# Kernel optimization log

Hardware: AMD Instinct MI355X
Metric: run time of the kernel (lower is better)

Reference implementation:

```python
import jax, jax.numpy as jnp
import numpy as np

CLS_NUM = 16
SCALE = 8.0
STRIDE = 5
NO_OBJ_SCALE = 1.0
EPS = 1e-7


def setup_inputs() -> dict:
    key = jax.random.key(0)
    k1, k2, k3, k4, k5, k6, k7, k8 = jax.random.split(key, 8)
    nB, nH, nW = 16, 160, 160
    N = 2048
    predict = jax.random.normal(k1, (nB, 6 + CLS_NUM, nH, nW), dtype=jnp.float32)
    b = jax.random.randint(k2, (N,), 0, nB).astype(jnp.float32)
    c = jax.random.randint(k3, (N,), 0, CLS_NUM).astype(jnp.float32)
    cx = jax.random.uniform(k4, (N,), minval=0.0, maxval=nW * SCALE)
    cy = jax.random.uniform(k5, (N,), minval=0.0, maxval=nH * SCALE)
    w = jax.random.uniform(k6, (N,), minval=8.0, maxval=80.0)
    h = jax.random.uniform(k7, (N,), minval=8.0, maxval=80.0)
    ang = jax.random.uniform(k8, (N,), minval=-np.pi, maxval=np.pi)
    targets = jnp.stack([b, c, cx, cy, w, h, ang], axis=-1).astype(jnp.float32)
    return {"predict": predict, "targets": targets}


def _masks(targets, nB, nH, nW):
    """Vectorized render_map/build_heatmap: per-(class,batch) obj / noobj grid masks."""
    b_idx = targets[:, 0].astype(jnp.int32)
    c_idx = targets[:, 1].astype(jnp.int32)
    cx = targets[:, 2] / SCALE
    cy = targets[:, 3] / SCALE
    w = targets[:, 4] / SCALE
    h = targets[:, 5] / SCALE
    ang = targets[:, 6]
    cos, sin = jnp.cos(ang), jnp.sin(ang)
    xr = cx * cos + cy * sin          # rotated box center
    yr = -cx * sin + cy * cos
    x3, x4 = xr - h / 2, xr + h / 2   # tight bounds
    y3, y4 = yr - w / 2, yr + w / 2
    x1, x2 = x3 - 0.5, x4 + 0.5       # widened bounds (noobj clearing)
    y1, y2 = y3 - 0.5, y4 + 0.5
    gx = jnp.arange(nW, dtype=jnp.float32) + 0.5   # [W]
    gy = jnp.arange(nH, dtype=jnp.float32) + 0.5   # [H]
    # rotated grid coords per box: [N, H, W]
    vx = cos[:, None, None] * gx[None, None, :] + sin[:, None, None] * gy[None, :, None]
    vy = -sin[:, None, None] * gx[None, None, :] + cos[:, None, None] * gy[None, :, None]

    def inside(xl, xh, yl, yh):
        m = (xl[:, None, None] <= vx) & (vx <= xh[:, None, None]) \
            & (yl[:, None, None] <= vy) & (vy <= yh[:, None, None])
        return m.astype(jnp.float32)

    obj_n = inside(x3, x4, y3, y4)    # [N, H, W]
    wide_n = inside(x1, x2, y1, y2)
    seg = c_idx * nB + b_idx
    nseg = CLS_NUM * nB
    obj_sum = jax.ops.segment_sum(obj_n, seg, num_segments=nseg).reshape(CLS_NUM, nB, nH, nW)
    wide_sum = jax.ops.segment_sum(wide_n, seg, num_segments=nseg).reshape(CLS_NUM, nB, nH, nW)
    obj_mask = obj_sum > 0
    noobj_mask = wide_sum == 0
    return obj_mask, noobj_mask


def reference(predict, targets):
    nB, C, nH, nW = predict.shape
    pred = jnp.transpose(predict, (0, 2, 3, 1))  # [B, H, W, C]
    half = (STRIDE - 1) / 2
    x = jax.nn.sigmoid(pred[..., 0]) * STRIDE - half
    y = jax.nn.sigmoid(pred[..., 1]) * STRIDE - half
    w = pred[..., 2]
    h = pred[..., 3]
    p = jax.nn.sigmoid(pred[..., 4]) * 2 - 1
    q = jax.nn.sigmoid(pred[..., 5]) * 2 - 1

    # ---- confidence loss (per class, BCE on obj / noobj cells) ----
    obj_mask, noobj_mask = _masks(targets, nB, nH, nW)     # [Cls, B, H, W]
    conf = jax.nn.sigmoid(jnp.transpose(pred[..., 6:], (3, 0, 1, 2)))  # [Cls, B, H, W]
    confc = jnp.clip(conf, EPS, 1.0 - EPS)
    obj_f = obj_mask.astype(conf.dtype)
    noobj_f = noobj_mask.astype(conf.dtype)
    n_obj = jnp.sum(obj_f, axis=(1, 2, 3))
    n_noobj = jnp.sum(noobj_f, axis=(1, 2, 3))
    loss_obj = jnp.sum(obj_f * (-jnp.log(confc)), axis=(1, 2, 3)) / jnp.maximum(n_obj, 1.0)
    loss_noobj = jnp.sum(noobj_f * (-jnp.log(1.0 - confc)), axis=(1, 2, 3)) / jnp.maximum(n_noobj, 1.0)
    per_cls = jnp.where(n_obj > 0, loss_obj + NO_OBJ_SCALE * loss_noobj, 0.0)
    loss = jnp.sum(per_cls)

    # ---- box decoding (eval output) ----
    score = jax.nn.sigmoid(pred[..., 6:])
    conf_max = jnp.max(score, axis=-1)
    cls_id = jnp.argmax(score, axis=-1).astype(pred.dtype)
    grid_x = jnp.broadcast_to(jnp.arange(nW, dtype=pred.dtype)[None, None, :], (nB, nH, nW))
    grid_y = jnp.broadcast_to(jnp.arange(nH, dtype=pred.dtype)[None, :, None], (nB, nH, nW))
    t = jnp.sqrt((1 + p) / 2 + 1e-16)
    bang = jnp.arctan2(q / (2 * t + 1e-16), t)
    boxes = jnp.stack([
        conf_max,
        cls_id,
        (grid_x + x) * SCALE,
        (grid_y + y) * SCALE,
        jnp.exp(w) * SCALE,
        jnp.exp(h) * SCALE,
        bang,
    ], axis=-1)                      # [B, H, W, 7]
    output = boxes.reshape(nB, nH * nW, 7)
    return (loss, output)
```

## Files before the change

kernel.cpp:

```cpp
#include <hip/hip_runtime.h>
#include <math.h>

#define CLS_NUM 16
#define NB 16
#define NH 160
#define NW 160
#define NCH 22
#define CSZ 25600
#define NT 2048
#define TPB 256
#define NBOXU 1600
#define NMASKU 2560
#define CAP 256
#define EPS_F 1e-7f


__global__ __launch_bounds__(TPB) void detect_main(
        const float* __restrict__ predict,
        const float* __restrict__ targets,
        float* __restrict__ out,
        float* __restrict__ partial)
{
    __shared__ float tg[CAP][6];
    __shared__ float red_s[16];
    __shared__ int cnt_s;

    const int tid = threadIdx.x;
    const int bid = blockIdx.x;

    if (bid < NBOXU) {
        int b = bid / 100;
        int r = (bid % 100) * TPB + tid;
        const float* pb = predict + (size_t)b * NCH * CSZ + r;
        float p0 = pb[0];
        float p1 = pb[1 * CSZ];
        float p2 = pb[2 * CSZ];
        float p3 = pb[3 * CSZ];
        float p4 = pb[4 * CSZ];
        float p5 = pb[5 * CSZ];
        float bestraw = pb[6 * CSZ];
        int bi = 0;
        #pragma unroll
        for (int cc = 1; cc < CLS_NUM; cc++) {
            float v = pb[(6 + cc) * CSZ];
            if (v > bestraw) { bestraw = v; bi = cc; }
        }
        float x = 1.0f / (1.0f + __expf(-p0)) * 5.0f - 2.0f;
        float y = 1.0f / (1.0f + __expf(-p1)) * 5.0f - 2.0f;
        float p = 1.0f / (1.0f + __expf(-p4)) * 2.0f - 1.0f;
        float q = 1.0f / (1.0f + __expf(-p5)) * 2.0f - 1.0f;
        float best = 1.0f / (1.0f + __expf(-bestraw));
        float tq = sqrtf((1.0f + p) * 0.5f + 1e-16f);
        float bang = atan2f(q / (2.0f * tq + 1e-16f), tq);
        int i = r / NW, j = r % NW;
        float* o = out + 1 + ((size_t)b * CSZ + r) * 7;
        o[0] = best;
        o[1] = (float)bi;
        o[2] = ((float)j + x) * 8.0f;
        o[3] = ((float)i + y) * 8.0f;
        o[4] = __expf(p2) * 8.0f;
        o[5] = __expf(p3) * 8.0f;
        o[6] = bang;
        return;
    }

    const int u = bid - NBOXU;
    const int pair = u / 10, tile = u - pair * 10;
    const int c = pair >> 4, b = pair & 15;
    const int rb = tile * 16;

    if (tid == 0) cnt_s = 0;
    __syncthreads();

    const float rbc = (float)rb + 8.0f;
    const float rlo = (float)rb + 0.5f, rhi = (float)rb + 15.5f;

    for (int n = tid; n < NT; n += TPB) {
        const float* tp = targets + n * 7;
        if ((int)tp[0] == b && (int)tp[1] == c) {
            float cx = tp[2] * 0.125f, cy = tp[3] * 0.125f;
            float w  = tp[4] * 0.125f, h  = tp[5] * 0.125f;
            float R = 0.5f * sqrtf(w * w + h * h) + 0.75f;
            if (cy + R >= rlo && cy - R <= rhi) {
                float ang = tp[6];
                float cs_ = cosf(ang), sn_ = sinf(ang);
                float xr =  cx * cs_ + cy * sn_;
                float yr = -cx * sn_ + cy * cs_;
                float x3 = xr - h * 0.5f, x4 = xr + h * 0.5f;
                float y3 = yr - w * 0.5f, y4 = yr + w * 0.5f;
                float acs = fabsf(cs_), asn = fabsf(sn_);
                float ex = acs * 79.5f + asn * 7.5f + 1e-3f;
                float ey = acs * 7.5f  + asn * 79.5f + 1e-3f;
                float vxc = cs_ * 80.0f + sn_ * rbc;
                float vyc = cs_ * rbc   - sn_ * 80.0f;
                if (!(vxc + ex < x3 - 0.5f || vxc - ex > x4 + 0.5f ||
                      vyc + ey < y3 - 0.5f || vyc - ey > y4 + 0.5f)) {
                    int slot = atomicAdd(&cnt_s, 1);
                    if (slot < CAP) {
                        tg[slot][0] = cs_; tg[slot][1] = sn_;
                        tg[slot][2] = x3;  tg[slot][3] = x4;
                        tg[slot][4] = y3;  tg[slot][5] = y4;
                    }
                }
            }
        }
    }
    __syncthreads();
    const int cnt = min(cnt_s, CAP);

    float gx[10], gy[10];
    #pragma unroll
    for (int k = 0; k < 10; k++) {
        int cell = tid + k * TPB;
        gx[k] = (float)(cell % NW) + 0.5f;
        gy[k] = (float)(rb + cell / NW) + 0.5f;
    }

    unsigned objb = 0, wideb = 0;
    for (int t = 0; t < cnt; t++) {
        float cs_ = tg[t][0], sn_ = tg[t][1];
        float x3 = tg[t][2], x4 = tg[t][3], y3 = tg[t][4], y4 = tg[t][5];
        #pragma unroll
        for (int k = 0; k < 10; k++) {
            float vx = cs_ * gx[k] + sn_ * gy[k];
            float vy = cs_ * gy[k] - sn_ * gx[k];
            float mn = fminf(fminf(vx - x3, x4 - vx),
                             fminf(vy - y3, y4 - vy));
            objb  |= (mn >= 0.0f)  ? (1u << k) : 0u;
            wideb |= (mn >= -0.5f) ? (1u << k) : 0u;
        }
    }

    const float* cp = predict + ((size_t)(b * NCH + 6 + c)) * CSZ + rb * NW;
    float ao = 0.f, an = 0.f;
    #pragma unroll
    for (int k = 0; k < 10; k++) {
        float pv = cp[tid + k * TPB];
        float s  = 1.0f / (1.0f + __expf(-pv));
        float sc = fminf(fmaxf(s, EPS_F), 1.0f - EPS_F);
        if ((objb >> k) & 1u)     ao -= __logf(sc);
        if (!((wideb >> k) & 1u)) an -= __logf(1.0f - sc);
    }
    float co = (float)__popc(objb);
    float cn = (float)__popc(~wideb & 0x3FFu);
    #pragma unroll
    for (int o = 32; o > 0; o >>= 1) {
        ao += __shfl_down(ao, o);
        an += __shfl_down(an, o);
        co += __shfl_down(co, o);
        cn += __shfl_down(cn, o);
    }
    if ((tid & 63) == 0) {
        int wid = tid >> 6;
        red_s[wid * 4 + 0] = ao; red_s[wid * 4 + 1] = an;
        red_s[wid * 4 + 2] = co; red_s[wid * 4 + 3] = cn;
    }
    __syncthreads();
    if (tid < 4) {
        float s = red_s[tid] + red_s[4 + tid] + red_s[8 + tid] + red_s[12 + tid];
        partial[u * 4 + tid] = s;
    }
}

__global__ __launch_bounds__(256) void finalize_kernel(
        const float* __restrict__ partial,
        float* __restrict__ out)
{
    __shared__ float fin_s[4][64];
    int tid = threadIdx.x;
    int v = tid & 63, g = tid >> 6;
    int c2 = v >> 2, comp = v & 3;
    float s = 0.f;
    for (int i = 0; i < 40; i++)
        s += partial[(c2 * 160 + g * 40 + i) * 4 + comp];
    fin_s[g][v] = s;
    __syncthreads();
    if (tid < 64)
        fin_s[0][tid] = fin_s[0][tid] + fin_s[1][tid] + fin_s[2][tid] + fin_s[3][tid];
    __syncthreads();
    if (tid == 0) {
        float L = 0.f;
        for (int c = 0; c < CLS_NUM; c++) {
            float ao = fin_s[0][c * 4 + 0], an = fin_s[0][c * 4 + 1];
            float co = fin_s[0][c * 4 + 2], cn = fin_s[0][c * 4 + 3];
            if (co > 0.f) L += ao / fmaxf(co, 1.f) + an / fmaxf(cn, 1.f);
        }
        out[0] = L;
    }
}

extern "C" void kernel_launch(void* const* d_in, const int* in_sizes, int n_in,
                              void* d_out, int out_size, void* d_ws, size_t ws_size,
                              hipStream_t stream) {
    const float* predict = (const float*)d_in[0];
    const float* targets = (const float*)d_in[1];
    float* out = (float*)d_out;
    float* partial = (float*)d_ws;

    detect_main<<<NBOXU + NMASKU, TPB, 0, stream>>>(predict, targets, out, partial);
    finalize_kernel<<<1, 256, 0, stream>>>(partial, out);
}
```

Measured before the change: 41.58 us.

## Fold noobj loss into box-decode pass and sparsify mask blocks across classes

```diff
diff --git a/kernel.cpp b/kernel.cpp
--- a/kernel.cpp
+++ b/kernel.cpp
@@ -10,7 +10,9 @@
 #define NT 2048
 #define TPB 256
 #define NBOXU 1600
-#define NMASKU 2560
+#define TILES 40
+#define NMASKU 640
+#define TCELLS 640
 #define CAP 256
 #define EPS_F 1e-7f
 
@@ -19,16 +21,17 @@
         const float* __restrict__ predict,
         const float* __restrict__ targets,
         float* __restrict__ out,
-        float* __restrict__ partial)
+        float* __restrict__ streamP,
+        float* __restrict__ maskP)
 {
-    __shared__ float tg[CAP][6];
-    __shared__ float red_s[16];
-    __shared__ int cnt_s;
-
     const int tid = threadIdx.x;
     const int bid = blockIdx.x;
 
     if (bid < NBOXU) {
+        __shared__ float acc_b[16];
+        if (tid < 16) acc_b[tid] = 0.f;
+        __syncthreads();
+
         int b = bid / 100;
         int r = (bid % 100) * TPB + tid;
         const float* pb = predict + (size_t)b * NCH * CSZ + r;
@@ -38,13 +41,25 @@
         float p3 = pb[3 * CSZ];
         float p4 = pb[4 * CSZ];
         float p5 = pb[5 * CSZ];
-        float bestraw = pb[6 * CSZ];
-        int bi = 0;
-        #pragma unroll
-        for (int cc = 1; cc < CLS_NUM; cc++) {
-            float v = pb[(6 + cc) * CSZ];
-            if (v > bestraw) { bestraw = v; bi = cc; }
-        }
+        float raw[16];
+        #pragma unroll
+        for (int cc = 0; cc < CLS_NUM; cc++) raw[cc] = pb[(6 + cc) * CSZ];
+
+        float bestraw = raw[0]; int bi = 0;
+        #pragma unroll
+        for (int cc = 1; cc < CLS_NUM; cc++)
+            if (raw[cc] > bestraw) { bestraw = raw[cc]; bi = cc; }
+
+        #pragma unroll
+        for (int cc = 0; cc < CLS_NUM; cc++) {
+            float s  = 1.0f / (1.0f + __expf(-raw[cc]));
+            float sc = fminf(fmaxf(s, EPS_F), 1.0f - EPS_F);
+            float v  = -__logf(1.0f - sc);
+            #pragma unroll
+            for (int o = 32; o > 0; o >>= 1) v += __shfl_down(v, o);
+            if ((tid & 63) == 0) atomicAdd(&acc_b[cc], v);
+        }
+
         float x = 1.0f / (1.0f + __expf(-p0)) * 5.0f - 2.0f;
         float y = 1.0f / (1.0f + __expf(-p1)) * 5.0f - 2.0f;
         float p = 1.0f / (1.0f + __expf(-p4)) * 2.0f - 1.0f;
@@ -61,27 +76,36 @@
         o[4] = __expf(p2) * 8.0f;
         o[5] = __expf(p3) * 8.0f;
         o[6] = bang;
+
+        __syncthreads();
+        if (tid < 16) streamP[bid * 16 + tid] = acc_b[tid];
         return;
     }
 
+    __shared__ float tg[CAP][8];
+    __shared__ float acc_s[64];
+    __shared__ int cnt_s, pres_s;
+
     const int u = bid - NBOXU;
-    const int pair = u / 10, tile = u - pair * 10;
-    const int c = pair >> 4, b = pair & 15;
-    const int rb = tile * 16;
-
-    if (tid == 0) cnt_s = 0;
-    __syncthreads();
-
-    const float rbc = (float)rb + 8.0f;
-    const float rlo = (float)rb + 0.5f, rhi = (float)rb + 15.5f;
+    const int b = u / TILES;
+    const int tile = u - b * TILES;
+    const int rb = tile * 4;
+
+    if (tid == 0) { cnt_s = 0; pres_s = 0; }
+    if (tid < 64) acc_s[tid] = 0.f;
+    __syncthreads();
+
+    const float rlo = (float)rb + 0.5f, rhi = (float)rb + 3.5f;
+    const float rbc = (float)rb + 2.0f;
 
     for (int n = tid; n < NT; n += TPB) {
         const float* tp = targets + n * 7;
-        if ((int)tp[0] == b && (int)tp[1] == c) {
-            float cx = tp[2] * 0.125f, cy = tp[3] * 0.125f;
-            float w  = tp[4] * 0.125f, h  = tp[5] * 0.125f;
+        if ((int)tp[0] == b) {
+            float cy = tp[3] * 0.125f;
+            float w  = tp[4] * 0.125f, h = tp[5] * 0.125f;
             float R = 0.5f * sqrtf(w * w + h * h) + 0.75f;
             if (cy + R >= rlo && cy - R <= rhi) {
+                float cx = tp[2] * 0.125f;
                 float ang = tp[6];
                 float cs_ = cosf(ang), sn_ = sinf(ang);
                 float xr =  cx * cs_ + cy * sn_;
@@ -89,8 +113,8 @@
                 float x3 = xr - h * 0.5f, x4 = xr + h * 0.5f;
                 float y3 = yr - w * 0.5f, y4 = yr + w * 0.5f;
                 float acs = fabsf(cs_), asn = fabsf(sn_);
-                float ex = acs * 79.5f + asn * 7.5f + 1e-3f;
-                float ey = acs * 7.5f  + asn * 79.5f + 1e-3f;
+                float ex = acs * 79.5f + asn * 1.5f + 1e-3f;
+                float ey = acs * 1.5f  + asn * 79.5f + 1e-3f;
                 float vxc = cs_ * 80.0f + sn_ * rbc;
                 float vyc = cs_ * rbc   - sn_ * 80.0f;
                 if (!(vxc + ex < x3 - 0.5f || vxc - ex > x4 + 0.5f ||
@@ -100,6 +124,7 @@
                         tg[slot][0] = cs_; tg[slot][1] = sn_;
                         tg[slot][2] = x3;  tg[slot][3] = x4;
                         tg[slot][4] = y3;  tg[slot][5] = y4;
+                        tg[slot][6] = tp[1];
                     }
                 }
             }
@@ -108,82 +133,115 @@
     __syncthreads();
     const int cnt = min(cnt_s, CAP);
 
-    float gx[10], gy[10];
+    float gxa[3], gya[3];
     #pragma unroll
-    for (int k = 0; k < 10; k++) {
+    for (int k = 0; k < 3; k++) {
         int cell = tid + k * TPB;
-        gx[k] = (float)(cell % NW) + 0.5f;
-        gy[k] = (float)(rb + cell / NW) + 0.5f;
-    }
-
-    unsigned objb = 0, wideb = 0;
+        gxa[k] = (float)(cell % NW) + 0.5f;
+        gya[k] = (float)(rb + cell / NW) + 0.5f;
+    }
+    unsigned m[3] = {0u, 0u, 0u};
     for (int t = 0; t < cnt; t++) {
         float cs_ = tg[t][0], sn_ = tg[t][1];
         float x3 = tg[t][2], x4 = tg[t][3], y3 = tg[t][4], y4 = tg[t][5];
-        #pragma unroll
-        for (int k = 0; k < 10; k++) {
-            float vx = cs_ * gx[k] + sn_ * gy[k];
-            float vy = cs_ * gy[k] - sn_ * gx[k];
-            float mn = fminf(fminf(vx - x3, x4 - vx),
-                             fminf(vy - y3, y4 - vy));
-            objb  |= (mn >= 0.0f)  ? (1u << k) : 0u;
-            wideb |= (mn >= -0.5f) ? (1u << k) : 0u;
-        }
-    }
-
-    const float* cp = predict + ((size_t)(b * NCH + 6 + c)) * CSZ + rb * NW;
-    float ao = 0.f, an = 0.f;
+        int cl = (int)tg[t][6];
+        #pragma unroll
+        for (int k = 0; k < 3; k++) {
+            float vx = cs_ * gxa[k] + sn_ * gya[k];
+            float vy = cs_ * gya[k] - sn_ * gxa[k];
+            float mn = fminf(fminf(vx - x3, x4 - vx), fminf(vy - y3, y4 - vy));
+            unsigned add = (mn >= 0.0f ? 1u : 0u) | (mn >= -0.5f ? 0x10000u : 0u);
+            m[k] |= add << cl;
+        }
+    }
+    if (tid >= TCELLS - 2 * TPB) m[2] = 0u;
+
+    unsigned any = m[0] | m[1] | m[2];
     #pragma unroll
-    for (int k = 0; k < 10; k++) {
-        float pv = cp[tid + k * TPB];
-        float s  = 1.0f / (1.0f + __expf(-pv));
-        float sc = fminf(fmaxf(s, EPS_F), 1.0f - EPS_F);
-        if ((objb >> k) & 1u)     ao -= __logf(sc);
-        if (!((wideb >> k) & 1u)) an -= __logf(1.0f - sc);
-    }
-    float co = (float)__popc(objb);
-    float cn = (float)__popc(~wideb & 0x3FFu);
-    #pragma unroll
-    for (int o = 32; o > 0; o >>= 1) {
-        ao += __shfl_down(ao, o);
-        an += __shfl_down(an, o);
-        co += __shfl_down(co, o);
-        cn += __shfl_down(cn, o);
-    }
-    if ((tid & 63) == 0) {
-        int wid = tid >> 6;
-        red_s[wid * 4 + 0] = ao; red_s[wid * 4 + 1] = an;
-        red_s[wid * 4 + 2] = co; red_s[wid * 4 + 3] = cn;
-    }
-    __syncthreads();
-    if (tid < 4) {
-        float s = red_s[tid] + red_s[4 + tid] + red_s[8 + tid] + red_s[12 + tid];
-        partial[u * 4 + tid] = s;
-    }
+    for (int o = 32; o > 0; o >>= 1) any |= (unsigned)__shfl_down((int)any, o);
+    if ((tid & 63) == 0) atomicOr(&pres_s, (int)any);
+    __syncthreads();
+    const unsigned pres = (unsigned)pres_s;
+
+    const float* basec = predict + ((size_t)b * NCH + 6) * CSZ + rb * NW;
+    for (int c = 0; c < CLS_NUM; c++) {
+        if (!(pres & (0x10000u << c))) continue;
+        const float* cp = basec + (size_t)c * CSZ;
+        float ao = 0.f, no = 0.f, wsub = 0.f, wc = 0.f;
+        #pragma unroll
+        for (int k = 0; k < 3; k++) {
+            int cell = tid + k * TPB;
+            bool ob = (m[k] >> c) & 1u;
+            bool wb = (m[k] >> (16 + c)) & 1u;
+            if ((ob | wb) && cell < TCELLS) {
+                float pv = cp[cell];
+                float s  = 1.0f / (1.0f + __expf(-pv));
+                float sc = fminf(fmaxf(s, EPS_F), 1.0f - EPS_F);
+                if (ob) { ao -= __logf(sc);        no += 1.0f; }
+                if (wb) { wsub -= __logf(1.0f - sc); wc += 1.0f; }
+            }
+        }
+        #pragma unroll
+        for (int o = 32; o > 0; o >>= 1) {
+            ao   += __shfl_down(ao, o);
+            no   += __shfl_down(no, o);
+            wsub += __shfl_down(wsub, o);
+            wc   += __shfl_down(wc, o);
+        }
+        if ((tid & 63) == 0) {
+            atomicAdd(&acc_s[c * 4 + 0], ao);
+            atomicAdd(&acc_s[c * 4 + 1], no);
+            atomicAdd(&acc_s[c * 4 + 2], wsub);
+            atomicAdd(&acc_s[c * 4 + 3], wc);
+        }
+    }
+    __syncthreads();
+    if (tid < 64) maskP[u * 64 + tid] = acc_s[tid];
 }
 
 __global__ __launch_bounds__(256) void finalize_kernel(
-        const float* __restrict__ partial,
+        const float* __restrict__ streamP,
+        const float* __restrict__ maskP,
         float* __restrict__ out)
 {
-    __shared__ float fin_s[4][64];
+    __shared__ float st[16][16];
+    __shared__ float mt[4][64];
+    __shared__ float S[16];
+    __shared__ float M[64];
     int tid = threadIdx.x;
-    int v = tid & 63, g = tid >> 6;
-    int c2 = v >> 2, comp = v & 3;
-    float s = 0.f;
-    for (int i = 0; i < 40; i++)
-        s += partial[(c2 * 160 + g * 40 + i) * 4 + comp];
-    fin_s[g][v] = s;
-    __syncthreads();
-    if (tid < 64)
-        fin_s[0][tid] = fin_s[0][tid] + fin_s[1][tid] + fin_s[2][tid] + fin_s[3][tid];
+    {   int g = tid >> 4, c = tid & 15;
+        float s = 0.f;
+        for (int blk = g * 100; blk < g * 100 + 100; blk++)
+            s += streamP[blk * 16 + c];
+        st[g][c] = s;
+    }
+    {   int g = tid >> 6, v = tid & 63;
+        float s = 0.f;
+        for (int uu = g; uu < NMASKU; uu += 4) s += maskP[uu * 64 + v];
+        mt[g][v] = s;
+    }
+    __syncthreads();
+    if (tid < 64) M[tid] = mt[0][tid] + mt[1][tid] + mt[2][tid] + mt[3][tid];
+    if (tid >= 64 && tid < 80) {
+        int c = tid - 64;
+        float s = 0.f;
+        #pragma unroll
+        for (int g = 0; g < 16; g++) s += st[g][c];
+        S[c] = s;
+    }
     __syncthreads();
     if (tid == 0) {
         float L = 0.f;
         for (int c = 0; c < CLS_NUM; c++) {
-            float ao = fin_s[0][c * 4 + 0], an = fin_s[0][c * 4 + 1];
-            float co = fin_s[0][c * 4 + 2], cn = fin_s[0][c * 4 + 3];
-            if (co > 0.f) L += ao / fmaxf(co, 1.f) + an / fmaxf(cn, 1.f);
+            float ao   = M[c * 4 + 0];
+            float no   = M[c * 4 + 1];
+            float wsub = M[c * 4 + 2];
+            float wc   = M[c * 4 + 3];
+            if (no > 0.f) {
+                float nnoobj = 409600.0f - wc;
+                L += ao / fmaxf(no, 1.0f)
+                   + (S[c] - wsub) / fmaxf(nnoobj, 1.0f);
+            }
         }
         out[0] = L;
     }
@@ -195,8 +253,11 @@
     const float* predict = (const float*)d_in[0];
     const float* targets = (const float*)d_in[1];
     float* out = (float*)d_out;
-    float* partial = (float*)d_ws;
-
-    detect_main<<<NBOXU + NMASKU, TPB, 0, stream>>>(predict, targets, out, partial);
-    finalize_kernel<<<1, 256, 0, stream>>>(partial, out);
+
+    float* streamP = (float*)d_ws;
+    float* maskP   = streamP + NBOXU * 16;
+
+    detect_main<<<NBOXU + NMASKU, TPB, 0, stream>>>(predict, targets, out,
+                                                    streamP, maskP);
+    finalize_kernel<<<1, 256, 0, stream>>>(streamP, maskP, out);
 }
```

New measurement: 82.46 us. 98.3% more time.

## Fuse box decoding and per-class mask loss into one banded kernel

Applied to the files above, without the earlier changes.

```diff
diff --git a/kernel.cpp b/kernel.cpp
--- a/kernel.cpp
+++ b/kernel.cpp
@@ -8,80 +8,44 @@
 #define NCH 22
 #define CSZ 25600
 #define NT 2048
-#define TPB 256
-#define NBOXU 1600
-#define NMASKU 2560
+#define TPB 320
+#define BANDS 40
+#define NU 640
+#define BCELLS 640
 #define CAP 256
 #define EPS_F 1e-7f
 
 
-__global__ __launch_bounds__(TPB) void detect_main(
+__global__ __launch_bounds__(TPB) void detect_unified(
         const float* __restrict__ predict,
         const float* __restrict__ targets,
         float* __restrict__ out,
-        float* __restrict__ partial)
+        float* __restrict__ maskP)
 {
-    __shared__ float tg[CAP][6];
-    __shared__ float red_s[16];
+    __shared__ float tg[CAP][8];
+    __shared__ float acc_s[64];
     __shared__ int cnt_s;
 
     const int tid = threadIdx.x;
-    const int bid = blockIdx.x;
-
-    if (bid < NBOXU) {
-        int b = bid / 100;
-        int r = (bid % 100) * TPB + tid;
-        const float* pb = predict + (size_t)b * NCH * CSZ + r;
-        float p0 = pb[0];
-        float p1 = pb[1 * CSZ];
-        float p2 = pb[2 * CSZ];
-        float p3 = pb[3 * CSZ];
-        float p4 = pb[4 * CSZ];
-        float p5 = pb[5 * CSZ];
-        float bestraw = pb[6 * CSZ];
-        int bi = 0;
-        #pragma unroll
-        for (int cc = 1; cc < CLS_NUM; cc++) {
-            float v = pb[(6 + cc) * CSZ];
-            if (v > bestraw) { bestraw = v; bi = cc; }
-        }
-        float x = 1.0f / (1.0f + __expf(-p0)) * 5.0f - 2.0f;
-        float y = 1.0f / (1.0f + __expf(-p1)) * 5.0f - 2.0f;
-        float p = 1.0f / (1.0f + __expf(-p4)) * 2.0f - 1.0f;
-        float q = 1.0f / (1.0f + __expf(-p5)) * 2.0f - 1.0f;
-        float best = 1.0f / (1.0f + __expf(-bestraw));
-        float tq = sqrtf((1.0f + p) * 0.5f + 1e-16f);
-        float bang = atan2f(q / (2.0f * tq + 1e-16f), tq);
-        int i = r / NW, j = r % NW;
-        float* o = out + 1 + ((size_t)b * CSZ + r) * 7;
-        o[0] = best;
-        o[1] = (float)bi;
-        o[2] = ((float)j + x) * 8.0f;
-        o[3] = ((float)i + y) * 8.0f;
-        o[4] = __expf(p2) * 8.0f;
-        o[5] = __expf(p3) * 8.0f;
-        o[6] = bang;
-        return;
-    }
-
-    const int u = bid - NBOXU;
-    const int pair = u / 10, tile = u - pair * 10;
-    const int c = pair >> 4, b = pair & 15;
-    const int rb = tile * 16;
+    const int u   = blockIdx.x;
+    const int b   = u / BANDS;
+    const int band = u - b * BANDS;
+    const int rb  = band * 4;
 
     if (tid == 0) cnt_s = 0;
-    __syncthreads();
-
-    const float rbc = (float)rb + 8.0f;
-    const float rlo = (float)rb + 0.5f, rhi = (float)rb + 15.5f;
-
+    if (tid < 64) acc_s[tid] = 0.f;
+    __syncthreads();
+
+    const float rlo = (float)rb + 0.5f, rhi = (float)rb + 3.5f;
+    const float rbc = (float)rb + 2.0f;
     for (int n = tid; n < NT; n += TPB) {
         const float* tp = targets + n * 7;
-        if ((int)tp[0] == b && (int)tp[1] == c) {
-            float cx = tp[2] * 0.125f, cy = tp[3] * 0.125f;
-            float w  = tp[4] * 0.125f, h  = tp[5] * 0.125f;
+        if ((int)tp[0] == b) {
+            float cy = tp[3] * 0.125f;
+            float w  = tp[4] * 0.125f, h = tp[5] * 0.125f;
             float R = 0.5f * sqrtf(w * w + h * h) + 0.75f;
             if (cy + R >= rlo && cy - R <= rhi) {
+                float cx = tp[2] * 0.125f;
                 float ang = tp[6];
                 float cs_ = cosf(ang), sn_ = sinf(ang);
                 float xr =  cx * cs_ + cy * sn_;
@@ -89,8 +53,8 @@
                 float x3 = xr - h * 0.5f, x4 = xr + h * 0.5f;
                 float y3 = yr - w * 0.5f, y4 = yr + w * 0.5f;
                 float acs = fabsf(cs_), asn = fabsf(sn_);
-                float ex = acs * 79.5f + asn * 7.5f + 1e-3f;
-                float ey = acs * 7.5f  + asn * 79.5f + 1e-3f;
+                float ex = acs * 79.5f + asn * 1.5f + 1e-3f;
+                float ey = acs * 1.5f  + asn * 79.5f + 1e-3f;
                 float vxc = cs_ * 80.0f + sn_ * rbc;
                 float vyc = cs_ * rbc   - sn_ * 80.0f;
                 if (!(vxc + ex < x3 - 0.5f || vxc - ex > x4 + 0.5f ||
@@ -100,6 +64,7 @@
                         tg[slot][0] = cs_; tg[slot][1] = sn_;
                         tg[slot][2] = x3;  tg[slot][3] = x4;
                         tg[slot][4] = y3;  tg[slot][5] = y4;
+                        tg[slot][6] = tp[1];
                     }
                 }
             }
@@ -108,82 +73,122 @@
     __syncthreads();
     const int cnt = min(cnt_s, CAP);
 
-    float gx[10], gy[10];
+    unsigned m0 = 0u, m1 = 0u;
+    {
+        float gx0 = (float)(tid % NW) + 0.5f;
+        float gy0 = (float)(rb + tid / NW) + 0.5f;
+        int cell1 = tid + TPB;
+        float gx1 = (float)(cell1 % NW) + 0.5f;
+        float gy1 = (float)(rb + cell1 / NW) + 0.5f;
+        for (int t = 0; t < cnt; t++) {
+            float cs_ = tg[t][0], sn_ = tg[t][1];
+            float x3 = tg[t][2], x4 = tg[t][3], y3 = tg[t][4], y4 = tg[t][5];
+            int cl = (int)tg[t][6];
+            float vx0 = cs_ * gx0 + sn_ * gy0;
+            float vy0 = cs_ * gy0 - sn_ * gx0;
+            float mn0 = fminf(fminf(vx0 - x3, x4 - vx0), fminf(vy0 - y3, y4 - vy0));
+            m0 |= ((mn0 >= 0.0f ? 1u : 0u) | (mn0 >= -0.5f ? 0x10000u : 0u)) << cl;
+            float vx1 = cs_ * gx1 + sn_ * gy1;
+            float vy1 = cs_ * gy1 - sn_ * gx1;
+            float mn1 = fminf(fminf(vx1 - x3, x4 - vx1), fminf(vy1 - y3, y4 - vy1));
+            m1 |= ((mn1 >= 0.0f ? 1u : 0u) | (mn1 >= -0.5f ? 0x10000u : 0u)) << cl;
+        }
+    }
+
+    const float* pbase = predict + (size_t)b * NCH * CSZ + rb * NW;
+    float anS[16];
     #pragma unroll
-    for (int k = 0; k < 10; k++) {
-        int cell = tid + k * TPB;
-        gx[k] = (float)(cell % NW) + 0.5f;
-        gy[k] = (float)(rb + cell / NW) + 0.5f;
-    }
-
-    unsigned objb = 0, wideb = 0;
-    for (int t = 0; t < cnt; t++) {
-        float cs_ = tg[t][0], sn_ = tg[t][1];
-        float x3 = tg[t][2], x4 = tg[t][3], y3 = tg[t][4], y4 = tg[t][5];
+    for (int c = 0; c < CLS_NUM; c++) anS[c] = 0.f;
+
+    #pragma unroll
+    for (int k = 0; k < 2; k++) {
+        const unsigned mk = k ? m1 : m0;
+        const int cell = tid + k * TPB;
+        float bestraw = -INFINITY;
+        int bi = 0;
         #pragma unroll
-        for (int k = 0; k < 10; k++) {
-            float vx = cs_ * gx[k] + sn_ * gy[k];
-            float vy = cs_ * gy[k] - sn_ * gx[k];
-            float mn = fminf(fminf(vx - x3, x4 - vx),
-                             fminf(vy - y3, y4 - vy));
-            objb  |= (mn >= 0.0f)  ? (1u << k) : 0u;
-            wideb |= (mn >= -0.5f) ? (1u << k) : 0u;
-        }
-    }
-
-    const float* cp = predict + ((size_t)(b * NCH + 6 + c)) * CSZ + rb * NW;
-    float ao = 0.f, an = 0.f;
+        for (int c = 0; c < CLS_NUM; c++) {
+            float pv = pbase[(size_t)(6 + c) * CSZ + cell];
+            if (pv > bestraw) { bestraw = pv; bi = c; }
+            float s  = 1.0f / (1.0f + __expf(-pv));
+            float sc = fminf(fmaxf(s, EPS_F), 1.0f - EPS_F);
+            float lnn = -__logf(1.0f - sc);
+            bool wb = (mk >> (16 + c)) & 1u;
+            bool ob = (mk >> c) & 1u;
+            anS[c] += wb ? 0.f : lnn;
+            if (ob) {
+                atomicAdd(&acc_s[c * 4 + 0], -__logf(sc));
+                atomicAdd(&acc_s[c * 4 + 1], 1.0f);
+            }
+            if (wb) atomicAdd(&acc_s[c * 4 + 3], 1.0f);
+        }
+        float p0 = pbase[cell];
+        float p1 = pbase[(size_t)1 * CSZ + cell];
+        float p2 = pbase[(size_t)2 * CSZ + cell];
+        float p3 = pbase[(size_t)3 * CSZ + cell];
+        float p4 = pbase[(size_t)4 * CSZ + cell];
+        float p5 = pbase[(size_t)5 * CSZ + cell];
+        float x = 1.0f / (1.0f + __expf(-p0)) * 5.0f - 2.0f;
+        float y = 1.0f / (1.0f + __expf(-p1)) * 5.0f - 2.0f;
+        float p = 1.0f / (1.0f + __expf(-p4)) * 2.0f - 1.0f;
+        float q = 1.0f / (1.0f + __expf(-p5)) * 2.0f - 1.0f;
+        float best = 1.0f / (1.0f + __expf(-bestraw));
+        float tq = sqrtf((1.0f + p) * 0.5f + 1e-16f);
+        float bang = atan2f(q / (2.0f * tq + 1e-16f), tq);
+        int i = rb + cell / NW, j = cell % NW;
+        float* o = out + 1 + ((size_t)b * CSZ + (size_t)i * NW + j) * 7;
+        o[0] = best;
+        o[1] = (float)bi;
+        o[2] = ((float)j + x) * 8.0f;
+        o[3] = ((float)i + y) * 8.0f;
+        o[4] = __expf(p2) * 8.0f;
+        o[5] = __expf(p3) * 8.0f;
+        o[6] = bang;
+    }
+
     #pragma unroll
-    for (int k = 0; k < 10; k++) {
-        float pv = cp[tid + k * TPB];
-        float s  = 1.0f / (1.0f + __expf(-pv));
-        float sc = fminf(fmaxf(s, EPS_F), 1.0f - EPS_F);
-        if ((objb >> k) & 1u)     ao -= __logf(sc);
-        if (!((wideb >> k) & 1u)) an -= __logf(1.0f - sc);
-    }
-    float co = (float)__popc(objb);
-    float cn = (float)__popc(~wideb & 0x3FFu);
-    #pragma unroll
-    for (int o = 32; o > 0; o >>= 1) {
-        ao += __shfl_down(ao, o);
-        an += __shfl_down(an, o);
-        co += __shfl_down(co, o);
-        cn += __shfl_down(cn, o);
-    }
-    if ((tid & 63) == 0) {
-        int wid = tid >> 6;
-        red_s[wid * 4 + 0] = ao; red_s[wid * 4 + 1] = an;
-        red_s[wid * 4 + 2] = co; red_s[wid * 4 + 3] = cn;
-    }
-    __syncthreads();
-    if (tid < 4) {
-        float s = red_s[tid] + red_s[4 + tid] + red_s[8 + tid] + red_s[12 + tid];
-        partial[u * 4 + tid] = s;
-    }
+    for (int c = 0; c < CLS_NUM; c++) {
+        float v = anS[c];
+        #pragma unroll
+        for (int o = 32; o > 0; o >>= 1) v += __shfl_down(v, o);
+        if ((tid & 63) == 0) atomicAdd(&acc_s[c * 4 + 2], v);
+    }
+    __syncthreads();
+    if (tid < 64) maskP[u * 64 + tid] = acc_s[tid];
 }
 
-__global__ __launch_bounds__(256) void finalize_kernel(
-        const float* __restrict__ partial,
+__global__ __launch_bounds__(1024) void finalize_kernel(
+        const float* __restrict__ maskP,
         float* __restrict__ out)
 {
-    __shared__ float fin_s[4][64];
-    int tid = threadIdx.x;
-    int v = tid & 63, g = tid >> 6;
-    int c2 = v >> 2, comp = v & 3;
+    __shared__ float fin[16][64];
+    __shared__ float M[64];
+    const int tid = threadIdx.x;
+    const int v = tid & 63;
+    const int g = tid >> 6;
     float s = 0.f;
-    for (int i = 0; i < 40; i++)
-        s += partial[(c2 * 160 + g * 40 + i) * 4 + comp];
-    fin_s[g][v] = s;
-    __syncthreads();
-    if (tid < 64)
-        fin_s[0][tid] = fin_s[0][tid] + fin_s[1][tid] + fin_s[2][tid] + fin_s[3][tid];
+    for (int i = tid; i < NU * 64; i += 1024)
+        s += maskP[i];
+    fin[g][v] = s;
+    __syncthreads();
+    if (tid < 64) {
+        float t = 0.f;
+        #pragma unroll
+        for (int gg = 0; gg < 16; gg++) t += fin[gg][tid];
+        M[tid] = t;
+    }
     __syncthreads();
     if (tid == 0) {
         float L = 0.f;
         for (int c = 0; c < CLS_NUM; c++) {
-            float ao = fin_s[0][c * 4 + 0], an = fin_s[0][c * 4 + 1];
-            float co = fin_s[0][c * 4 + 2], cn = fin_s[0][c * 4 + 3];
-            if (co > 0.f) L += ao / fmaxf(co, 1.f) + an / fmaxf(cn, 1.f);
+            float ao = M[c * 4 + 0];
+            float no = M[c * 4 + 1];
+            float an = M[c * 4 + 2];
+            float wc = M[c * 4 + 3];
+            if (no > 0.f) {
+                float nn = 409600.0f - wc;
+                L += ao / fmaxf(no, 1.0f) + an / fmaxf(nn, 1.0f);
+            }
         }
         out[0] = L;
     }
@@ -195,8 +200,8 @@
     const float* predict = (const float*)d_in[0];
     const float* targets = (const float*)d_in[1];
     float* out = (float*)d_out;
-    float* partial = (float*)d_ws;
-
-    detect_main<<<NBOXU + NMASKU, TPB, 0, stream>>>(predict, targets, out, partial);
-    finalize_kernel<<<1, 256, 0, stream>>>(partial, out);
+    float* maskP = (float*)d_ws;
+
+    detect_unified<<<NU, TPB, 0, stream>>>(predict, targets, out, maskP);
+    finalize_kernel<<<1, 1024, 0, stream>>>(maskP, out);
 }
```

Result: slower. 52.00 us (+25.1%).
